# Optimization experiments

Measured on AMD Instinct MI355X. Metric: run time of the kernel, lower is better.

Reference implementation:

```python
import jax, jax.numpy as jnp
import numpy as np

B, N, E, H, R, L, VOCAB, KINDS = 8, 4096, 524288, 128, 8, 2, 100000, 8


def setup_inputs() -> dict:
    key = jax.random.key(0)
    ks = jax.random.split(key, 12)
    concept_ids = jax.random.randint(ks[0], (B, N), 1, VOCAB)  # avoid padding_idx 0
    kind_ids = jax.random.randint(ks[1], (B, N), 0, KINDS)
    node_mask = jnp.ones((B, N), dtype=jnp.int32)
    # edges constrained within each batch block (module assumes per-subgraph edges)
    e_batch = jax.random.randint(ks[2], (E,), 0, B)
    src = e_batch * N + jax.random.randint(ks[3], (E,), 0, N)
    dst = e_batch * N + jax.random.randint(ks[4], (E,), 0, N)
    edge_index = jnp.stack([src, dst], axis=0)
    edge_type = jax.random.randint(ks[5], (E,), 0, R)
    s = 0.02
    concept_emb = jax.random.normal(ks[6], (VOCAB, H), jnp.float32) * s
    concept_emb = concept_emb.at[0].set(0.0)  # padding_idx=0
    kind_emb = jax.random.normal(ks[7], (KINDS, H), jnp.float32) * s
    proj_W = jax.random.normal(ks[8], (H, H), jnp.float32) * s
    proj_b = jnp.zeros((H,), jnp.float32)
    self_W = jax.random.normal(ks[9], (L, H, H), jnp.float32) * s
    self_b = jnp.zeros((L, H), jnp.float32)
    rel_W = jax.random.normal(ks[10], (L, R, H, H), jnp.float32) * s
    return dict(pkg_node_concept_ids=concept_ids, pkg_node_kind_ids=kind_ids,
                pkg_node_mask=node_mask, pkg_edge_index=edge_index,
                pkg_edge_type=edge_type, concept_emb=concept_emb, kind_emb=kind_emb,
                proj_W=proj_W, proj_b=proj_b, self_W=self_W, self_b=self_b, rel_W=rel_W)


def reference(pkg_node_concept_ids, pkg_node_kind_ids, pkg_node_mask,
              pkg_edge_index, pkg_edge_type, concept_emb, kind_emb,
              proj_W, proj_b, self_W, self_b, rel_W):
    b, n = pkg_node_concept_ids.shape
    num_nodes = b * n
    # input embedding + projection (dropout = identity in eval)
    x = concept_emb[pkg_node_concept_ids] + kind_emb[pkg_node_kind_ids]  # [B,N,H]
    x = jnp.einsum('bnh,gh->bng', x, proj_W) + proj_b
    x = x.reshape(num_nodes, -1)  # packed node states [B*N, H]
    src, dst = pkg_edge_index[0], pkg_edge_index[1]
    deg = jax.ops.segment_sum(jnp.ones_like(src, dtype=x.dtype), dst,
                              num_segments=num_nodes)[:, None]
    deg = jnp.maximum(deg, 1.0)
    n_layers, n_rel = rel_W.shape[0], rel_W.shape[1]
    for l in range(n_layers):
        xs = x[src]  # [E,H] gather
        msgs = jnp.zeros_like(xs)
        for r in range(n_rel):
            msgs = msgs + jnp.where((pkg_edge_type == r)[:, None],
                                    xs @ rel_W[l, r].T, 0.0)
        agg = jax.ops.segment_sum(msgs, dst, num_segments=num_nodes) / deg
        x = jax.nn.relu(x @ self_W[l].T + self_b[l] + agg)
    out = x.reshape(b, n, -1) * pkg_node_mask[..., None].astype(x.dtype)
    return out
```

## Files before the change

### kernel.cpp

```cpp
#include <hip/hip_runtime.h>
#include <hip/hip_bf16.h>

#define NODES 32768
#define HD 128
#define NE 524288
#define NR 8

typedef unsigned int u32;
typedef unsigned short u16;
typedef __attribute__((ext_vector_type(8))) short bf16x8;
typedef __attribute__((ext_vector_type(4))) float f32x4;

#define XH_OFF   (0u)
#define XL_OFF   (8u<<20)
#define Y_OFF    (16u<<20)
#define Z_OFF    (80u<<20)
#define ADJ_OFF  (96u<<20)
#define RP_OFF   (98u<<20)
#define CUR_OFF  ((98u<<20)+(256u<<10))
#define BSUM_OFF ((98u<<20)+(512u<<10))
#define BP_OFF   ((98u<<20)+(640u<<10))

#define BP_LAYER 294912
#define PP_ELEM  589824

__device__ __forceinline__ float bflo(u32 u){ union{u32 i;float f;}c; c.i=u<<16; return c.f; }
__device__ __forceinline__ float bfhi(u32 u){ union{u32 i;float f;}c; c.i=u&0xffff0000u; return c.f; }
__device__ __forceinline__ u16 f2bf(float f){
  u32 u=__float_as_uint(f);
  u32 r=u + 0x7fffu + ((u>>16)&1u);
  return (u16)(r>>16);
}
__device__ __forceinline__ float bf2f(u16 h){ return __uint_as_float(((u32)h)<<16); }

__device__ __forceinline__ void gl_lds16(const void* g, void* l){
  __builtin_amdgcn_global_load_lds((const __attribute__((address_space(1))) u32*)g,
                                   (__attribute__((address_space(3))) u32*)l, 16, 0, 0);
}

__global__ void prep_w(const float* __restrict__ rW, const float* __restrict__ sW,
                       const float* __restrict__ pWg, u16* __restrict__ Bp)
{
  int idx=blockIdx.x*256+threadIdx.x;
  if(idx<294912){
    int l=idx/147456;
    int rem=idx%147456;
    int t=rem>>14;
    int kn=rem&16383;
    int k=kn>>7, n=kn&127;
    float w;
    if(t<8) w=rW[(((size_t)l*NR+t)*HD+n)*HD+k];
    else    w=sW[((size_t)l*HD+n)*HD+k];
    u16* base=Bp+(size_t)l*BP_LAYER+(size_t)t*32768;
    int ks=k>>5, q=(k>>3)&3, j=k&7;
    size_t off=((size_t)ks*128+n)*32+q*8+j;
    u16 hb=f2bf(w);
    u16 lb=f2bf(w-bf2f(hb));
    base[off]=hb;
    base[off+16384]=lb;
  } else {
    int kn=idx-294912;
    int k=kn>>7, n=kn&127;
    float w=pWg[(size_t)n*HD+k];
    u16* base=Bp+PP_ELEM;
    int ks=k>>5, q=(k>>3)&3, j=k&7;
    size_t off=((size_t)ks*128+n)*32+q*8+j;
    u16 hb=f2bf(w);
    u16 lb=f2bf(w-bf2f(hb));
    base[off]=hb;
    base[off+16384]=lb;
  }
}

__global__ __launch_bounds__(256,2) void embed_mfma(
    const int* __restrict__ cid, const int* __restrict__ kid,
    const float* __restrict__ cemb, const float* __restrict__ kemb,
    const u16* __restrict__ PP, const float* __restrict__ pb,
    u16* __restrict__ xh, u16* __restrict__ xl)
{
  __shared__ u16 Atile[2][128*128];
  const int tid=threadIdx.x;
  const int wave=tid>>6, lane=tid&63;
  const int wm=wave>>1, wn=wave&1;
  const int q=lane>>4;
  const int d0=blockIdx.x*128;

  { int r=tid>>1, half=tid&1;
    int ci=cid[d0+r], ki=kid[d0+r];
    const float* cp=cemb+(size_t)ci*HD+half*64;
    const float* kp=kemb+(size_t)ki*HD+half*64;
#pragma unroll
    for(int cc=0;cc<8;cc++){
      float4 a0=*(const float4*)(cp+cc*8);
      float4 a1=*(const float4*)(cp+cc*8+4);
      float4 b0=*(const float4*)(kp+cc*8);
      float4 b1=*(const float4*)(kp+cc*8+4);
      float v[8]={a0.x+b0.x,a0.y+b0.y,a0.z+b0.z,a0.w+b0.w,
                  a1.x+b1.x,a1.y+b1.y,a1.z+b1.z,a1.w+b1.w};
      u16 hb[8], lb[8];
#pragma unroll
      for(int j=0;j<8;j++){ hb[j]=f2bf(v[j]); lb[j]=f2bf(v[j]-bf2f(hb[j])); }
      int chunk=half*8+cc;
      int dst=r*128+(chunk^(r&15))*8;
      uint4 hv={(u32)hb[0]|((u32)hb[1]<<16),(u32)hb[2]|((u32)hb[3]<<16),
                (u32)hb[4]|((u32)hb[5]<<16),(u32)hb[6]|((u32)hb[7]<<16)};
      uint4 lv={(u32)lb[0]|((u32)lb[1]<<16),(u32)lb[2]|((u32)lb[3]<<16),
                (u32)lb[4]|((u32)lb[5]<<16),(u32)lb[6]|((u32)lb[7]<<16)};
      *(uint4*)&Atile[0][dst]=hv;
      *(uint4*)&Atile[1][dst]=lv;
    }
  }
  __syncthreads();

  f32x4 acc[4][4];
#pragma unroll
  for(int a=0;a<4;a++)
#pragma unroll
    for(int b=0;b<4;b++) acc[a][b]=(f32x4){0.f,0.f,0.f,0.f};

#pragma unroll
  for(int ks=0;ks<4;ks++){
    bf16x8 ah[4];
#pragma unroll
    for(int tm=0;tm<4;tm++){
      int m=wm*64+tm*16+(lane&15);
      ah[tm]=*(const bf16x8*)&Atile[0][m*128+(((ks*4)+q)^(m&15))*8];
    }
#pragma unroll
    for(int s=0;s<2;s++){
      const u16* Bb=PP+s*16384;
#pragma unroll
      for(int tn=0;tn<4;tn++){
        int n=wn*64+tn*16+(lane&15);
        bf16x8 bfr=*(const bf16x8*)&Bb[((size_t)ks*128+n)*32+q*8];
#pragma unroll
        for(int tm=0;tm<4;tm++)
          acc[tm][tn]=__builtin_amdgcn_mfma_f32_16x16x32_bf16(ah[tm],bfr,acc[tm][tn],0,0,0);
      }
    }
  }
#pragma unroll
  for(int ks=0;ks<4;ks++){
    bf16x8 al[4];
#pragma unroll
    for(int tm=0;tm<4;tm++){
      int m=wm*64+tm*16+(lane&15);
      al[tm]=*(const bf16x8*)&Atile[1][m*128+(((ks*4)+q)^(m&15))*8];
    }
#pragma unroll
    for(int tn=0;tn<4;tn++){
      int n=wn*64+tn*16+(lane&15);
      bf16x8 bfr=*(const bf16x8*)&PP[((size_t)ks*128+n)*32+q*8];
#pragma unroll
      for(int tm=0;tm<4;tm++)
        acc[tm][tn]=__builtin_amdgcn_mfma_f32_16x16x32_bf16(al[tm],bfr,acc[tm][tn],0,0,0);
    }
  }

#pragma unroll
  for(int tn=0;tn<4;tn++){
    int n=wn*64+tn*16+(lane&15);
    float b=pb[n];
#pragma unroll
    for(int tm=0;tm<4;tm++){
      int rbase=d0+wm*64+tm*16+q*4;
#pragma unroll
      for(int r=0;r<4;r++){
        float v=acc[tm][tn][r]+b;
        u16 hb=f2bf(v);
        u16 lb=f2bf(v-bf2f(hb));
        xh[(size_t)(rbase+r)*HD+n]=hb;
        xl[(size_t)(rbase+r)*HD+n]=lb;
      }
    }
  }
}

__global__ void count_deg(const int* __restrict__ dst, u32* __restrict__ cnt){
  int e=blockIdx.x*256+threadIdx.x;
  atomicAdd(&cnt[dst[e]],1u);
}

__global__ void scan1(u32* __restrict__ cnt, u32* __restrict__ rp, u32* __restrict__ bsum){
  __shared__ u32 sh[256];
  int t=threadIdx.x; int base=blockIdx.x*256;
  u32 v=cnt[base+t]; sh[t]=v;
  cnt[base+t]=0u;
  __syncthreads();
  for(int off=1;off<256;off<<=1){
    u32 tv=(t>=off)?sh[t-off]:0u; __syncthreads();
    sh[t]+=tv; __syncthreads();
  }
  rp[base+t]=sh[t]-v;
  if(t==255) bsum[blockIdx.x]=sh[255];
}

__global__ void scan2(u32* __restrict__ bsum, u32* __restrict__ rp){
  __shared__ u32 sh[128];
  int t=threadIdx.x;
  u32 v=bsum[t]; sh[t]=v; __syncthreads();
  for(int off=1;off<128;off<<=1){
    u32 tv=(t>=off)?sh[t-off]:0u; __syncthreads();
    sh[t]+=tv; __syncthreads();
  }
  bsum[t]=sh[t]-v;
  if(t==0){ rp[NODES]=NE; bsum[128]=0u; }
}

__global__ void scatter_edges(const int* __restrict__ src, const int* __restrict__ dst,
                              const int* __restrict__ et, const u32* __restrict__ rp,
                              const u32* __restrict__ bsum,
                              u32* __restrict__ cur, u32* __restrict__ adj){
  int e=blockIdx.x*256+threadIdx.x;
  int d=dst[e];
  u32 pos=atomicAdd(&cur[d],1u);
  adj[rp[d]+bsum[d>>8]+pos]=(u32)(et[e]*NODES+src[e]);
}

__global__ __launch_bounds__(256,4) void gemm_y(
    const u16* __restrict__ xhi, const u16* __restrict__ xlo,
    const u16* __restrict__ Bt, u16* __restrict__ y, float* __restrict__ z)
{
  __shared__ u16 Atile[2][64*128];
  const int tid=threadIdx.x;
  const int wave=tid>>6, lane=tid&63;
  const int q=lane>>4;
  const int d0=blockIdx.x*64;
  const int t=blockIdx.y;
  const u16* Btile=Bt+(size_t)t*32768;

  const int st_c  = lane&15;
  const int st_rin= lane>>4;

#pragma unroll
  for(int i=0;i<4;i++){
    int rbase=wave*16+i*4;
    int r=rbase+st_rin;
    int g=st_c ^ (r&15);
    gl_lds16(xhi+(size_t)(d0+r)*HD+g*8, &Atile[0][rbase*128]);
  }
#pragma unroll
  for(int i=0;i<4;i++){
    int rbase=wave*16+i*4;
    int r=rbase+st_rin;
    int g=st_c ^ (r&15);
    gl_lds16(xlo+(size_t)(d0+r)*HD+g*8, &Atile[1][rbase*128]);
  }
  __syncthreads();

  f32x4 acc[4][2];
#pragma unroll
  for(int a=0;a<4;a++)
#pragma unroll
    for(int b=0;b<2;b++) acc[a][b]=(f32x4){0.f,0.f,0.f,0.f};

#pragma unroll
  for(int ks=0;ks<4;ks++){
    bf16x8 ah[4];
#pragma unroll
    for(int tm=0;tm<4;tm++){
      int m=tm*16+(lane&15);
      ah[tm]=*(const bf16x8*)&Atile[0][m*128+(((ks*4)+q)^(m&15))*8];
    }
#pragma unroll
    for(int s=0;s<2;s++){
      const u16* Bb=Btile+s*16384;
#pragma unroll
      for(int tn=0;tn<2;tn++){
        int n=wave*32+tn*16+(lane&15);
        bf16x8 bfr=*(const bf16x8*)&Bb[((size_t)ks*128+n)*32+q*8];
#pragma unroll
        for(int tm=0;tm<4;tm++)
          acc[tm][tn]=__builtin_amdgcn_mfma_f32_16x16x32_bf16(ah[tm],bfr,acc[tm][tn],0,0,0);
      }
    }
  }
#pragma unroll
  for(int ks=0;ks<4;ks++){
    bf16x8 al[4];
#pragma unroll
    for(int tm=0;tm<4;tm++){
      int m=tm*16+(lane&15);
      al[tm]=*(const bf16x8*)&Atile[1][m*128+(((ks*4)+q)^(m&15))*8];
    }
#pragma unroll
    for(int tn=0;tn<2;tn++){
      int n=wave*32+tn*16+(lane&15);
      bf16x8 bfr=*(const bf16x8*)&Btile[((size_t)ks*128+n)*32+q*8];
#pragma unroll
      for(int tm=0;tm<4;tm++)
        acc[tm][tn]=__builtin_amdgcn_mfma_f32_16x16x32_bf16(al[tm],bfr,acc[tm][tn],0,0,0);
    }
  }

  if(t<8){
    u16* yt=y+((size_t)t*NODES+d0)*HD;
#pragma unroll
    for(int tn=0;tn<2;tn++){
      int n=wave*32+tn*16+(lane&15);
#pragma unroll
      for(int tm=0;tm<4;tm++){
        int rbase=tm*16+q*4;
#pragma unroll
        for(int r=0;r<4;r++)
          yt[(size_t)(rbase+r)*HD+n]=f2bf(acc[tm][tn][r]);
      }
    }
  } else {
    float* zt=z+(size_t)d0*HD;
#pragma unroll
    for(int tn=0;tn<2;tn++){
      int n=wave*32+tn*16+(lane&15);
#pragma unroll
      for(int tm=0;tm<4;tm++){
        int rbase=tm*16+q*4;
#pragma unroll
        for(int r=0;r<4;r++)
          zt[(size_t)(rbase+r)*HD+n]=acc[tm][tn][r];
      }
    }
  }
}

__global__ __launch_bounds__(256) void gather_combine(
    const uint2* __restrict__ yy, const float* __restrict__ z,
    const u32* __restrict__ adj, const u32* __restrict__ rp, const u32* __restrict__ bsum,
    const float* __restrict__ sb, const int* __restrict__ mask,
    u32* __restrict__ xh, u32* __restrict__ xl, float* __restrict__ outf, int last)
{
  const int wave=threadIdx.x>>6, lane=threadIdx.x&63;
  const int node=blockIdx.x*4+wave;
  const int sub=lane>>5, c=lane&31;
  const int beg=(int)(rp[node]+bsum[node>>8]);
  const int end=(int)(rp[node+1]+bsum[(node+1)>>8]);
  float a0=0.f,a1=0.f,a2=0.f,a3=0.f;

  for(int base=beg; base<end; base+=64){
    int nk=end-base; if(nk>64) nk=64;
    u32 adjv = (lane<nk) ? adj[base+lane] : 0u;
    int i=0;
    for(; i+16<=nk; i+=16){
      uint2 vv[8];
#pragma unroll
      for(int j=0;j<8;j++){
        u32 row=(u32)__shfl((int)adjv, i+j*2+sub);
        vv[j]=yy[(size_t)row*32+c];
      }
#pragma unroll
      for(int j=0;j<8;j++){
        a0+=bflo(vv[j].x); a1+=bfhi(vv[j].x);
        a2+=bflo(vv[j].y); a3+=bfhi(vv[j].y);
      }
    }
    for(; i+2<=nk; i+=2){
      u32 row=(u32)__shfl((int)adjv, i+sub);
      uint2 v=yy[(size_t)row*32+c];
      a0+=bflo(v.x); a1+=bfhi(v.x); a2+=bflo(v.y); a3+=bfhi(v.y);
    }
    if(i<nk){
      u32 row=(u32)__shfl((int)adjv, i);
      if(sub==0){
        uint2 v=yy[(size_t)row*32+c];
        a0+=bflo(v.x); a1+=bfhi(v.x); a2+=bflo(v.y); a3+=bfhi(v.y);
      }
    }
  }

  a0+=__shfl_xor(a0,32); a1+=__shfl_xor(a1,32);
  a2+=__shfl_xor(a2,32); a3+=__shfl_xor(a3,32);

  if(sub==0){
    float inv=1.f/fmaxf((float)(end-beg),1.f);
    float4 zz=*(const float4*)&z[(size_t)node*HD+c*4];
    float4 bb=*(const float4*)&sb[c*4];
    float v0=fmaxf(zz.x+a0*inv+bb.x,0.f);
    float v1=fmaxf(zz.y+a1*inv+bb.y,0.f);
    float v2=fmaxf(zz.z+a2*inv+bb.z,0.f);
    float v3=fmaxf(zz.w+a3*inv+bb.w,0.f);
    if(last){
      float mk=(float)mask[node];
      float4 o={v0*mk,v1*mk,v2*mk,v3*mk};
      *(float4*)&outf[(size_t)node*HD+c*4]=o;
    } else {
      u16 h0=f2bf(v0), h1=f2bf(v1), h2=f2bf(v2), h3=f2bf(v3);
      u16 l0=f2bf(v0-bf2f(h0)), l1=f2bf(v1-bf2f(h1));
      u16 l2=f2bf(v2-bf2f(h2)), l3=f2bf(v3-bf2f(h3));
      uint2 hv={(u32)h0|((u32)h1<<16),(u32)h2|((u32)h3<<16)};
      uint2 lv={(u32)l0|((u32)l1<<16),(u32)l2|((u32)l3<<16)};
      *(uint2*)&xh[(size_t)node*64+c*2]=hv;
      *(uint2*)&xl[(size_t)node*64+c*2]=lv;
    }
  }
}

extern "C" void kernel_launch(void* const* d_in, const int* in_sizes, int n_in,
                              void* d_out, int out_size, void* d_ws, size_t ws_size,
                              hipStream_t stream)
{
  (void)in_sizes; (void)n_in; (void)out_size; (void)ws_size;
  const int*   cid =(const int*)  d_in[0];
  const int*   kid =(const int*)  d_in[1];
  const int*   mask=(const int*)  d_in[2];
  const int*   ei  =(const int*)  d_in[3];
  const int*   et  =(const int*)  d_in[4];
  const float* cemb=(const float*)d_in[5];
  const float* kemb=(const float*)d_in[6];
  const float* pW  =(const float*)d_in[7];
  const float* pb  =(const float*)d_in[8];
  const float* sW  =(const float*)d_in[9];
  const float* sb  =(const float*)d_in[10];
  const float* rW  =(const float*)d_in[11];
  float* out=(float*)d_out;
  char*  ws =(char*)d_ws;

  u16* xh =(u16*)(ws+XH_OFF);
  u16* xl =(u16*)(ws+XL_OFF);
  u16* y  =(u16*)(ws+Y_OFF);
  float* z=(float*)(ws+Z_OFF);
  u32* adj =(u32*)(ws+ADJ_OFF);
  u32* rp  =(u32*)(ws+RP_OFF);
  u32* cur =(u32*)(ws+CUR_OFF);
  u32* bsum=(u32*)(ws+BSUM_OFF);
  u16* Bp  =(u16*)(ws+BP_OFF);
  const int* srcA=ei;
  const int* dstA=ei+NE;

  hipMemsetAsync(cur,0,NODES*sizeof(u32),stream);
  prep_w<<<1216,256,0,stream>>>(rW,sW,pW,Bp);
  embed_mfma<<<NODES/128,256,0,stream>>>(cid,kid,cemb,kemb,Bp+PP_ELEM,pb,xh,xl);
  count_deg<<<NE/256,256,0,stream>>>(dstA,cur);
  scan1<<<NODES/256,256,0,stream>>>(cur,rp,bsum);
  scan2<<<1,128,0,stream>>>(bsum,rp);
  scatter_edges<<<NE/256,256,0,stream>>>(srcA,dstA,et,rp,bsum,cur,adj);

  gemm_y<<<dim3(NODES/64,9),256,0,stream>>>(xh,xl,Bp,y,z);
  gather_combine<<<NODES/4,256,0,stream>>>((const uint2*)y,z,adj,rp,bsum,sb,mask,(u32*)xh,(u32*)xl,out,0);
  gemm_y<<<dim3(NODES/64,9),256,0,stream>>>(xh,xl,Bp+BP_LAYER,y,z);
  gather_combine<<<NODES/4,256,0,stream>>>((const uint2*)y,z,adj,rp,bsum,sb+HD,mask,(u32*)xh,(u32*)xl,out,1);
}
```

Before: 308.6 us.

## Fuse gather-then-transform per layer: aggregate per relation, then MFMA in one kernel

Each layer no longer precomputes per-relation transforms for all nodes (a 9-way GEMM into a large bf16 Y buffer plus an fp32 Z buffer) followed by a gather. A single fused kernel first sums neighbour features per (node, relation) into LDS, then multiplies them by the relation weights with MFMA, adds the self transform, and applies the bias, degree normalisation and ReLU in registers. The edge CSR is re-keyed by (relation pair, dst, relation parity) so each pass covers two relations, and dst/parity are packed into the adjacency word. This removes the large intermediate writes and reads, but the gather now reads hi+lo bf16 node states, and the row-flush logic adds branches and small scattered LDS writes.

```diff
diff --git a/kernel.cpp b/kernel.cpp
--- a/kernel.cpp
+++ b/kernel.cpp
@@ -5,6 +5,8 @@
 #define HD 128
 #define NE 524288
 #define NR 8
+#define NS 262144
+#define PASSB 65536
 
 typedef unsigned int u32;
 typedef unsigned short u16;
@@ -13,13 +15,13 @@
 
 #define XH_OFF   (0u)
 #define XL_OFF   (8u<<20)
-#define Y_OFF    (16u<<20)
-#define Z_OFF    (80u<<20)
-#define ADJ_OFF  (96u<<20)
-#define RP_OFF   (98u<<20)
-#define CUR_OFF  ((98u<<20)+(256u<<10))
-#define BSUM_OFF ((98u<<20)+(512u<<10))
-#define BP_OFF   ((98u<<20)+(640u<<10))
+#define XH2_OFF  (16u<<20)
+#define XL2_OFF  (24u<<20)
+#define ADJ_OFF  (32u<<20)
+#define RP_OFF   (34u<<20)
+#define CUR_OFF  (36u<<20)
+#define BSUM_OFF (37u<<20)
+#define BP_OFF   (38u<<20)
 
 #define BP_LAYER 294912
 #define PP_ELEM  589824
@@ -176,9 +178,12 @@
   }
 }
 
-__global__ void count_deg(const int* __restrict__ dst, u32* __restrict__ cnt){
+__global__ void count_deg2(const int* __restrict__ dst, const int* __restrict__ et,
+                           u32* __restrict__ cnt){
   int e=blockIdx.x*256+threadIdx.x;
-  atomicAdd(&cnt[dst[e]],1u);
+  int t=et[e];
+  int key=(t>>1)*PASSB + dst[e]*2 + (t&1);
+  atomicAdd(&cnt[key],1u);
 }
 
 __global__ void scan1(u32* __restrict__ cnt, u32* __restrict__ rp, u32* __restrict__ bsum){
@@ -195,200 +200,228 @@
   if(t==255) bsum[blockIdx.x]=sh[255];
 }
 
-__global__ void scan2(u32* __restrict__ bsum, u32* __restrict__ rp){
-  __shared__ u32 sh[128];
+__global__ void scan2b(u32* __restrict__ bsum, u32* __restrict__ rp){
+  __shared__ u32 sh[256];
   int t=threadIdx.x;
-  u32 v=bsum[t]; sh[t]=v; __syncthreads();
-  for(int off=1;off<128;off<<=1){
+  u32 v0=bsum[t*4+0],v1=bsum[t*4+1],v2=bsum[t*4+2],v3=bsum[t*4+3];
+  u32 s=v0+v1+v2+v3;
+  sh[t]=s; __syncthreads();
+  for(int off=1;off<256;off<<=1){
     u32 tv=(t>=off)?sh[t-off]:0u; __syncthreads();
     sh[t]+=tv; __syncthreads();
   }
-  bsum[t]=sh[t]-v;
-  if(t==0){ rp[NODES]=NE; bsum[128]=0u; }
-}
-
-__global__ void scatter_edges(const int* __restrict__ src, const int* __restrict__ dst,
-                              const int* __restrict__ et, const u32* __restrict__ rp,
-                              const u32* __restrict__ bsum,
-                              u32* __restrict__ cur, u32* __restrict__ adj){
+  u32 ex=sh[t]-s;
+  bsum[t*4+0]=ex; bsum[t*4+1]=ex+v0; bsum[t*4+2]=ex+v0+v1; bsum[t*4+3]=ex+v0+v1+v2;
+  if(t==0) rp[NS]=NE;
+  if(t==255) bsum[1024]=0u;
+}
+
+__global__ void scatter_edges2(const int* __restrict__ src, const int* __restrict__ dst,
+                               const int* __restrict__ et, const u32* __restrict__ rp,
+                               const u32* __restrict__ bsum,
+                               u32* __restrict__ cur, u32* __restrict__ adj){
   int e=blockIdx.x*256+threadIdx.x;
+  int t=et[e];
   int d=dst[e];
-  u32 pos=atomicAdd(&cur[d],1u);
-  adj[rp[d]+bsum[d>>8]+pos]=(u32)(et[e]*NODES+src[e]);
-}
-
-__global__ __launch_bounds__(256,4) void gemm_y(
-    const u16* __restrict__ xhi, const u16* __restrict__ xlo,
-    const u16* __restrict__ Bt, u16* __restrict__ y, float* __restrict__ z)
+  int key=(t>>1)*PASSB + d*2 + (t&1);
+  u32 pos=atomicAdd(&cur[key],1u);
+  u32 val=(u32)src[e] | (((u32)(((t&1)<<5)|(d&31)))<<15);
+  adj[rp[key]+bsum[key>>8]+pos]=val;
+}
+
+#define FLUSHROW(rw,a0,a1) do{ \
+  u16 fh0=f2bf(a0), fh1=f2bf(a1); \
+  u16 fl0=f2bf((a0)-bf2f(fh0)), fl1=f2bf((a1)-bf2f(fh1)); \
+  int fw=(rw)*64 + (((lane>>2)^((rw)&15))<<2) + (lane&3); \
+  ((u32*)As[0])[fw]=(u32)fh0|((u32)fh1<<16); \
+  ((u32*)As[1])[fw]=(u32)fl0|((u32)fl1<<16); \
+}while(0)
+
+__global__ __launch_bounds__(256,4) void fused_layer(
+    const u16* __restrict__ xh, const u16* __restrict__ xl,
+    const u16* __restrict__ Bp,
+    const u32* __restrict__ rp, const u32* __restrict__ bsum,
+    const u32* __restrict__ adj,
+    const float* __restrict__ sb, const int* __restrict__ mask,
+    u16* __restrict__ oh, u16* __restrict__ ol, float* __restrict__ outf, int last)
 {
-  __shared__ u16 Atile[2][64*128];
+  __shared__ u16 As[2][64*128];
+  __shared__ float sdeg[32];
   const int tid=threadIdx.x;
   const int wave=tid>>6, lane=tid&63;
   const int q=lane>>4;
-  const int d0=blockIdx.x*64;
-  const int t=blockIdx.y;
-  const u16* Btile=Bt+(size_t)t*32768;
-
-  const int st_c  = lane&15;
-  const int st_rin= lane>>4;
-
-#pragma unroll
-  for(int i=0;i<4;i++){
-    int rbase=wave*16+i*4;
-    int r=rbase+st_rin;
-    int g=st_c ^ (r&15);
-    gl_lds16(xhi+(size_t)(d0+r)*HD+g*8, &Atile[0][rbase*128]);
-  }
-#pragma unroll
-  for(int i=0;i<4;i++){
-    int rbase=wave*16+i*4;
-    int r=rbase+st_rin;
-    int g=st_c ^ (r&15);
-    gl_lds16(xlo+(size_t)(d0+r)*HD+g*8, &Atile[1][rbase*128]);
+  const int d0=blockIdx.x*32;
+  const u32* xh32=(const u32*)xh;
+  const u32* xl32=(const u32*)xl;
+
+  f32x4 accR[2][2], accS[2][2];
+#pragma unroll
+  for(int a=0;a<2;a++)
+#pragma unroll
+    for(int b=0;b<2;b++){ accR[a][b]=(f32x4){0.f,0.f,0.f,0.f}; accS[a][b]=(f32x4){0.f,0.f,0.f,0.f}; }
+
+  for(int p=0;p<4;p++){
+    { uint4 zz={0u,0u,0u,0u};
+#pragma unroll
+      for(int rl=0;rl<2;rl++)
+#pragma unroll
+        for(int i=0;i<2;i++){
+          int row=rl*32+wave*8+i*4+(lane>>4);
+          int col16=lane&15;
+          *(uint4*)&As[0][row*128+col16*8]=zz;
+          *(uint4*)&As[1][row*128+col16*8]=zz;
+        }
+    }
+    { u32 k0=(u32)(p*PASSB + (d0+wave*8)*2);
+      u32 begW=rp[k0]+bsum[k0>>8];
+      u32 k1=k0+16;
+      u32 endW=rp[k1]+bsum[k1>>8];
+      int currow=-1; float v0=0.f,v1=0.f;
+      for(u32 base=begW; base<endW; base+=64){
+        int nk=(int)(endW-base); if(nk>64) nk=64;
+        u32 adjv=(lane<nk)?adj[base+lane]:0u;
+        int i=0;
+        for(; i+4<=nk; i+=4){
+          u32 w0=(u32)__shfl((int)adjv,i+0);
+          u32 w1=(u32)__shfl((int)adjv,i+1);
+          u32 w2=(u32)__shfl((int)adjv,i+2);
+          u32 w3=(u32)__shfl((int)adjv,i+3);
+          u32 h0=xh32[(size_t)(w0&0x7fffu)*64+lane], l0=xl32[(size_t)(w0&0x7fffu)*64+lane];
+          u32 h1=xh32[(size_t)(w1&0x7fffu)*64+lane], l1=xl32[(size_t)(w1&0x7fffu)*64+lane];
+          u32 h2=xh32[(size_t)(w2&0x7fffu)*64+lane], l2=xl32[(size_t)(w2&0x7fffu)*64+lane];
+          u32 h3=xh32[(size_t)(w3&0x7fffu)*64+lane], l3=xl32[(size_t)(w3&0x7fffu)*64+lane];
+          int r0=(int)(w0>>15);
+          if(r0!=currow){ if(currow>=0) FLUSHROW(currow,v0,v1); currow=r0; v0=0.f; v1=0.f; }
+          v0+=bflo(h0)+bflo(l0); v1+=bfhi(h0)+bfhi(l0);
+          int r1=(int)(w1>>15);
+          if(r1!=currow){ FLUSHROW(currow,v0,v1); currow=r1; v0=0.f; v1=0.f; }
+          v0+=bflo(h1)+bflo(l1); v1+=bfhi(h1)+bfhi(l1);
+          int r2=(int)(w2>>15);
+          if(r2!=currow){ FLUSHROW(currow,v0,v1); currow=r2; v0=0.f; v1=0.f; }
+          v0+=bflo(h2)+bflo(l2); v1+=bfhi(h2)+bfhi(l2);
+          int r3=(int)(w3>>15);
+          if(r3!=currow){ FLUSHROW(currow,v0,v1); currow=r3; v0=0.f; v1=0.f; }
+          v0+=bflo(h3)+bflo(l3); v1+=bfhi(h3)+bfhi(l3);
+        }
+        for(; i<nk; i++){
+          u32 w0=(u32)__shfl((int)adjv,i);
+          u32 h=xh32[(size_t)(w0&0x7fffu)*64+lane], l=xl32[(size_t)(w0&0x7fffu)*64+lane];
+          int r0=(int)(w0>>15);
+          if(r0!=currow){ if(currow>=0) FLUSHROW(currow,v0,v1); currow=r0; v0=0.f; v1=0.f; }
+          v0+=bflo(h)+bflo(l); v1+=bfhi(h)+bfhi(l);
+        }
+      }
+      if(currow>=0) FLUSHROW(currow,v0,v1);
+    }
+    __syncthreads();
+#pragma unroll
+    for(int rl=0;rl<2;rl++){
+      const u16* Bt=Bp+(size_t)(p*2+rl)*32768;
+#pragma unroll
+      for(int ks=0;ks<4;ks++){
+        bf16x8 ah[2],al[2];
+#pragma unroll
+        for(int mf=0;mf<2;mf++){
+          int ar=rl*32+mf*16+(lane&15);
+          int off=ar*128+((((ks<<2)+q)^(ar&15))<<3);
+          ah[mf]=*(const bf16x8*)&As[0][off];
+          al[mf]=*(const bf16x8*)&As[1][off];
+        }
+#pragma unroll
+        for(int tn=0;tn<2;tn++){
+          int n=wave*32+tn*16+(lane&15);
+          size_t boff=((size_t)(ks*128+n))*32+q*8;
+          bf16x8 bh=*(const bf16x8*)&Bt[boff];
+          bf16x8 bl=*(const bf16x8*)&Bt[boff+16384];
+#pragma unroll
+          for(int mf=0;mf<2;mf++){
+            accR[mf][tn]=__builtin_amdgcn_mfma_f32_16x16x32_bf16(ah[mf],bh,accR[mf][tn],0,0,0);
+            accR[mf][tn]=__builtin_amdgcn_mfma_f32_16x16x32_bf16(al[mf],bh,accR[mf][tn],0,0,0);
+            accR[mf][tn]=__builtin_amdgcn_mfma_f32_16x16x32_bf16(ah[mf],bl,accR[mf][tn],0,0,0);
+          }
+        }
+      }
+    }
+    __syncthreads();
+  }
+
+#pragma unroll
+  for(int i=0;i<2;i++){
+    int rbase=wave*8+i*4;
+    int r=rbase+(lane>>4);
+    int g=(lane&15)^(r&15);
+    gl_lds16(xh+(size_t)(d0+r)*HD+g*8, &As[0][rbase*128]);
+  }
+#pragma unroll
+  for(int i=0;i<2;i++){
+    int rbase=wave*8+i*4;
+    int r=rbase+(lane>>4);
+    int g=(lane&15)^(r&15);
+    gl_lds16(xl+(size_t)(d0+r)*HD+g*8, &As[1][rbase*128]);
+  }
+  if(tid<32){
+    int g=d0+tid; u32 dg=0;
+#pragma unroll
+    for(int ph=0;ph<4;ph++){
+      u32 k=(u32)(ph*PASSB+g*2);
+      dg+=(rp[k+2]+bsum[(k+2)>>8])-(rp[k]+bsum[k>>8]);
+    }
+    sdeg[tid]=1.f/fmaxf((float)dg,1.f);
   }
   __syncthreads();
-
-  f32x4 acc[4][2];
-#pragma unroll
-  for(int a=0;a<4;a++)
-#pragma unroll
-    for(int b=0;b<2;b++) acc[a][b]=(f32x4){0.f,0.f,0.f,0.f};
-
-#pragma unroll
-  for(int ks=0;ks<4;ks++){
-    bf16x8 ah[4];
-#pragma unroll
-    for(int tm=0;tm<4;tm++){
-      int m=tm*16+(lane&15);
-      ah[tm]=*(const bf16x8*)&Atile[0][m*128+(((ks*4)+q)^(m&15))*8];
-    }
-#pragma unroll
-    for(int s=0;s<2;s++){
-      const u16* Bb=Btile+s*16384;
+  { const u16* Bt=Bp+(size_t)8*32768;
+#pragma unroll
+    for(int ks=0;ks<4;ks++){
+      bf16x8 ah[2],al[2];
+#pragma unroll
+      for(int mf=0;mf<2;mf++){
+        int ar=mf*16+(lane&15);
+        int off=ar*128+((((ks<<2)+q)^(ar&15))<<3);
+        ah[mf]=*(const bf16x8*)&As[0][off];
+        al[mf]=*(const bf16x8*)&As[1][off];
+      }
 #pragma unroll
       for(int tn=0;tn<2;tn++){
         int n=wave*32+tn*16+(lane&15);
-        bf16x8 bfr=*(const bf16x8*)&Bb[((size_t)ks*128+n)*32+q*8];
-#pragma unroll
-        for(int tm=0;tm<4;tm++)
-          acc[tm][tn]=__builtin_amdgcn_mfma_f32_16x16x32_bf16(ah[tm],bfr,acc[tm][tn],0,0,0);
-      }
-    }
-  }
-#pragma unroll
-  for(int ks=0;ks<4;ks++){
-    bf16x8 al[4];
-#pragma unroll
-    for(int tm=0;tm<4;tm++){
-      int m=tm*16+(lane&15);
-      al[tm]=*(const bf16x8*)&Atile[1][m*128+(((ks*4)+q)^(m&15))*8];
-    }
-#pragma unroll
-    for(int tn=0;tn<2;tn++){
-      int n=wave*32+tn*16+(lane&15);
-      bf16x8 bfr=*(const bf16x8*)&Btile[((size_t)ks*128+n)*32+q*8];
-#pragma unroll
-      for(int tm=0;tm<4;tm++)
-        acc[tm][tn]=__builtin_amdgcn_mfma_f32_16x16x32_bf16(al[tm],bfr,acc[tm][tn],0,0,0);
-    }
-  }
-
-  if(t<8){
-    u16* yt=y+((size_t)t*NODES+d0)*HD;
-#pragma unroll
-    for(int tn=0;tn<2;tn++){
-      int n=wave*32+tn*16+(lane&15);
-#pragma unroll
-      for(int tm=0;tm<4;tm++){
-        int rbase=tm*16+q*4;
-#pragma unroll
-        for(int r=0;r<4;r++)
-          yt[(size_t)(rbase+r)*HD+n]=f2bf(acc[tm][tn][r]);
-      }
-    }
-  } else {
-    float* zt=z+(size_t)d0*HD;
-#pragma unroll
-    for(int tn=0;tn<2;tn++){
-      int n=wave*32+tn*16+(lane&15);
-#pragma unroll
-      for(int tm=0;tm<4;tm++){
-        int rbase=tm*16+q*4;
-#pragma unroll
-        for(int r=0;r<4;r++)
-          zt[(size_t)(rbase+r)*HD+n]=acc[tm][tn][r];
-      }
-    }
-  }
-}
-
-__global__ __launch_bounds__(256) void gather_combine(
-    const uint2* __restrict__ yy, const float* __restrict__ z,
-    const u32* __restrict__ adj, const u32* __restrict__ rp, const u32* __restrict__ bsum,
-    const float* __restrict__ sb, const int* __restrict__ mask,
-    u32* __restrict__ xh, u32* __restrict__ xl, float* __restrict__ outf, int last)
-{
-  const int wave=threadIdx.x>>6, lane=threadIdx.x&63;
-  const int node=blockIdx.x*4+wave;
-  const int sub=lane>>5, c=lane&31;
-  const int beg=(int)(rp[node]+bsum[node>>8]);
-  const int end=(int)(rp[node+1]+bsum[(node+1)>>8]);
-  float a0=0.f,a1=0.f,a2=0.f,a3=0.f;
-
-  for(int base=beg; base<end; base+=64){
-    int nk=end-base; if(nk>64) nk=64;
-    u32 adjv = (lane<nk) ? adj[base+lane] : 0u;
-    int i=0;
-    for(; i+16<=nk; i+=16){
-      uint2 vv[8];
-#pragma unroll
-      for(int j=0;j<8;j++){
-        u32 row=(u32)__shfl((int)adjv, i+j*2+sub);
-        vv[j]=yy[(size_t)row*32+c];
-      }
-#pragma unroll
-      for(int j=0;j<8;j++){
-        a0+=bflo(vv[j].x); a1+=bfhi(vv[j].x);
-        a2+=bflo(vv[j].y); a3+=bfhi(vv[j].y);
-      }
-    }
-    for(; i+2<=nk; i+=2){
-      u32 row=(u32)__shfl((int)adjv, i+sub);
-      uint2 v=yy[(size_t)row*32+c];
-      a0+=bflo(v.x); a1+=bfhi(v.x); a2+=bflo(v.y); a3+=bfhi(v.y);
-    }
-    if(i<nk){
-      u32 row=(u32)__shfl((int)adjv, i);
-      if(sub==0){
-        uint2 v=yy[(size_t)row*32+c];
-        a0+=bflo(v.x); a1+=bfhi(v.x); a2+=bflo(v.y); a3+=bfhi(v.y);
-      }
-    }
-  }
-
-  a0+=__shfl_xor(a0,32); a1+=__shfl_xor(a1,32);
-  a2+=__shfl_xor(a2,32); a3+=__shfl_xor(a3,32);
-
-  if(sub==0){
-    float inv=1.f/fmaxf((float)(end-beg),1.f);
-    float4 zz=*(const float4*)&z[(size_t)node*HD+c*4];
-    float4 bb=*(const float4*)&sb[c*4];
-    float v0=fmaxf(zz.x+a0*inv+bb.x,0.f);
-    float v1=fmaxf(zz.y+a1*inv+bb.y,0.f);
-    float v2=fmaxf(zz.z+a2*inv+bb.z,0.f);
-    float v3=fmaxf(zz.w+a3*inv+bb.w,0.f);
+        size_t boff=((size_t)(ks*128+n))*32+q*8;
+        bf16x8 bh=*(const bf16x8*)&Bt[boff];
+        bf16x8 bl=*(const bf16x8*)&Bt[boff+16384];
+#pragma unroll
+        for(int mf=0;mf<2;mf++){
+          accS[mf][tn]=__builtin_amdgcn_mfma_f32_16x16x32_bf16(ah[mf],bh,accS[mf][tn],0,0,0);
+          accS[mf][tn]=__builtin_amdgcn_mfma_f32_16x16x32_bf16(al[mf],bh,accS[mf][tn],0,0,0);
+          accS[mf][tn]=__builtin_amdgcn_mfma_f32_16x16x32_bf16(ah[mf],bl,accS[mf][tn],0,0,0);
+        }
+      }
+    }
+  }
+
+#pragma unroll
+  for(int tn=0;tn<2;tn++){
+    int n=wave*32+tn*16+(lane&15);
+    float bb=sb[n];
     if(last){
-      float mk=(float)mask[node];
-      float4 o={v0*mk,v1*mk,v2*mk,v3*mk};
-      *(float4*)&outf[(size_t)node*HD+c*4]=o;
+#pragma unroll
+      for(int mf=0;mf<2;mf++)
+#pragma unroll
+        for(int rr=0;rr<4;rr++){
+          int row=mf*16+q*4+rr;
+          float v=fmaxf(accS[mf][tn][rr]+bb+accR[mf][tn][rr]*sdeg[row],0.f);
+          v*=(float)mask[d0+row];
+          outf[(size_t)(d0+row)*HD+n]=v;
+        }
     } else {
-      u16 h0=f2bf(v0), h1=f2bf(v1), h2=f2bf(v2), h3=f2bf(v3);
-      u16 l0=f2bf(v0-bf2f(h0)), l1=f2bf(v1-bf2f(h1));
-      u16 l2=f2bf(v2-bf2f(h2)), l3=f2bf(v3-bf2f(h3));
-      uint2 hv={(u32)h0|((u32)h1<<16),(u32)h2|((u32)h3<<16)};
-      uint2 lv={(u32)l0|((u32)l1<<16),(u32)l2|((u32)l3<<16)};
-      *(uint2*)&xh[(size_t)node*64+c*2]=hv;
-      *(uint2*)&xl[(size_t)node*64+c*2]=lv;
+#pragma unroll
+      for(int mf=0;mf<2;mf++)
+#pragma unroll
+        for(int rr=0;rr<4;rr++){
+          int row=mf*16+q*4+rr;
+          float v=fmaxf(accS[mf][tn][rr]+bb+accR[mf][tn][rr]*sdeg[row],0.f);
+          u16 hb=f2bf(v);
+          u16 lb=f2bf(v-bf2f(hb));
+          oh[(size_t)(d0+row)*HD+n]=hb;
+          ol[(size_t)(d0+row)*HD+n]=lb;
+        }
     }
   }
 }
@@ -415,8 +448,8 @@
 
   u16* xh =(u16*)(ws+XH_OFF);
   u16* xl =(u16*)(ws+XL_OFF);
-  u16* y  =(u16*)(ws+Y_OFF);
-  float* z=(float*)(ws+Z_OFF);
+  u16* xh2=(u16*)(ws+XH2_OFF);
+  u16* xl2=(u16*)(ws+XL2_OFF);
   u32* adj =(u32*)(ws+ADJ_OFF);
   u32* rp  =(u32*)(ws+RP_OFF);
   u32* cur =(u32*)(ws+CUR_OFF);
@@ -425,16 +458,14 @@
   const int* srcA=ei;
   const int* dstA=ei+NE;
 
-  hipMemsetAsync(cur,0,NODES*sizeof(u32),stream);
+  hipMemsetAsync(cur,0,NS*sizeof(u32),stream);
   prep_w<<<1216,256,0,stream>>>(rW,sW,pW,Bp);
   embed_mfma<<<NODES/128,256,0,stream>>>(cid,kid,cemb,kemb,Bp+PP_ELEM,pb,xh,xl);
-  count_deg<<<NE/256,256,0,stream>>>(dstA,cur);
-  scan1<<<NODES/256,256,0,stream>>>(cur,rp,bsum);
-  scan2<<<1,128,0,stream>>>(bsum,rp);
-  scatter_edges<<<NE/256,256,0,stream>>>(srcA,dstA,et,rp,bsum,cur,adj);
-
-  gemm_y<<<dim3(NODES/64,9),256,0,stream>>>(xh,xl,Bp,y,z);
-  gather_combine<<<NODES/4,256,0,stream>>>((const uint2*)y,z,adj,rp,bsum,sb,mask,(u32*)xh,(u32*)xl,out,0);
-  gemm_y<<<dim3(NODES/64,9),256,0,stream>>>(xh,xl,Bp+BP_LAYER,y,z);
-  gather_combine<<<NODES/4,256,0,stream>>>((const uint2*)y,z,adj,rp,bsum,sb+HD,mask,(u32*)xh,(u32*)xl,out,1);
-}
+  count_deg2<<<NE/256,256,0,stream>>>(dstA,et,cur);
+  scan1<<<NS/256,256,0,stream>>>(cur,rp,bsum);
+  scan2b<<<1,256,0,stream>>>(bsum,rp);
+  scatter_edges2<<<NE/256,256,0,stream>>>(srcA,dstA,et,rp,bsum,cur,adj);
+
+  fused_layer<<<NODES/32,256,0,stream>>>(xh,xl,Bp,rp,bsum,adj,sb,mask,xh2,xl2,out,0);
+  fused_layer<<<NODES/32,256,0,stream>>>(xh2,xl2,Bp+BP_LAYER,rp,bsum,adj,sb+HD,mask,xh,xl,out,1);
+}
```

Result: slower. 317.2 us (+2.8%).
